# Optimization experiments

Measured on AMD Instinct MI355X. Metric: run time of the kernel, lower is better.

## Reference

```python
import jax, jax.numpy as jnp
import numpy as np

N = 50000
E = 800000
IN_DIM = 128
OUT_DIM = 64


def setup_inputs() -> dict:
    key = jax.random.key(0)
    ks = jax.random.split(key, 6)
    adj = jax.random.randint(ks[0], (2, E), 0, N)
    h = jax.random.normal(ks[1], (N, IN_DIM), dtype=jnp.float32)
    # fc: Linear(in_dim, out_dim) -> weight [out_dim, in_dim], bias [out_dim]
    W_fc = jax.random.normal(ks[2], (OUT_DIM, IN_DIM), dtype=jnp.float32) * (1.0 / np.sqrt(IN_DIM))
    b_fc = jnp.zeros((OUT_DIM,), dtype=jnp.float32)
    # attn_fc: Linear(2*out_dim, 1) -> weight [1, 2*out_dim], bias [1]
    W_att = jax.random.normal(ks[3], (1, 2 * OUT_DIM), dtype=jnp.float32) * (1.0 / np.sqrt(2 * OUT_DIM))
    b_att = jnp.zeros((1,), dtype=jnp.float32)
    return {"adj": adj, "h": h, "W_fc": W_fc, "b_fc": b_fc, "W_att": W_att, "b_att": b_att}


def reference(adj, h, W_fc, b_fc, W_att, b_att):
    # z = fc(h): [N, out_dim]
    z = h @ W_fc.T + b_fc
    src = adj[0]
    dst = adj[1]
    z_src = z[src]  # [E, out_dim]
    z_dst = z[dst]  # [E, out_dim]
    # attn_fc(cat(z_src, z_dst)) == z_src @ W1 + z_dst @ W2 + b; avoid explicit concat split
    w1 = W_att[0, :OUT_DIM]
    w2 = W_att[0, OUT_DIM:]
    att_logit = z_src @ w1 + z_dst @ w2 + b_att[0]  # [E]
    att_edge = jax.nn.leaky_relu(att_logit, negative_slope=0.01)[:, None]  # [E, 1]
    # scatter-add weighted source features to destination nodes
    out = jax.ops.segment_sum(z_src * att_edge, dst, num_segments=N)  # [N, out_dim]
    return out
```

## Files before the change

### kernel.cpp

```cpp
#include <hip/hip_runtime.h>
#include <hip/hip_bf16.h>

#define N_NODES 50000
#define E_EDGES 800000
#define IN_DIM  128
#define OUT_DIM 64
#define MTILES  (N_NODES / 16)
#define NB      196
#define BCAP    6144
#define OVF_CAP 16384
#define NBLK_FC 782
#define NBLK_SA 625
#define EPA     1280
#define ITER_A  5

static_assert(N_NODES % 16 == 0, "16-row MFMA tiles");
static_assert(N_NODES < 65536, "node ids packed in 16 bits");
static_assert(NBLK_SA * EPA == E_EDGES, "pass-A blocks partition edges");
static_assert(EPA == ITER_A * 256, "uniform per-thread trip count");
static_assert(NB * 256 >= N_NODES, "buckets cover dst space");


typedef __attribute__((ext_vector_type(8))) short bf16x8;
typedef __attribute__((ext_vector_type(4))) float f32x4;
typedef __attribute__((ext_vector_type(8))) unsigned short u16x8;

__device__ __forceinline__ unsigned short f32_to_bf16_rne(float f) {
    unsigned u = __float_as_uint(f);
    return (unsigned short)((u + 0x7FFFu + ((u >> 16) & 1u)) >> 16);
}
__device__ __forceinline__ float bf16_to_f32(unsigned short s) {
    return __uint_as_float(((unsigned)s) << 16);
}

__global__ __launch_bounds__(256) void gat_fc_scatter(
    const float* __restrict__ h,
    const float* __restrict__ Wfc,
    const float* __restrict__ bfc,
    const float* __restrict__ Watt,
    const float* __restrict__ batt,
    const int*   __restrict__ adj,
    unsigned short* __restrict__ z16,
    float* __restrict__ s1,
    float* __restrict__ s2,
    int*      __restrict__ gcnt,
    unsigned* __restrict__ coarse,
    unsigned* __restrict__ ovf)
{
    __shared__ short Wlds[OUT_DIM][IN_DIM + 8];

    if (blockIdx.x < NBLK_FC) {
        for (int i = threadIdx.x; i < OUT_DIM * IN_DIM; i += 256) {
            const int o = i >> 7;
            const int k = i & 127;
            Wlds[o][k] = (short)f32_to_bf16_rne(Wfc[i]);
        }
        __syncthreads();

        const int lane  = threadIdx.x & 63;
        const int c     = lane & 15;
        const int q     = lane >> 4;
        const int mtile = blockIdx.x * 4 + (threadIdx.x >> 6);
        if (mtile >= MTILES) return;
        const int n0 = mtile * 16;

        bf16x8 B[4][4];
        #pragma unroll
        for (int t = 0; t < 4; ++t)
            #pragma unroll
            for (int f = 0; f < 4; ++f)
                B[t][f] = *(const bf16x8*)&Wlds[f * 16 + c][t * 32 + q * 8];

        f32x4 acc[4] = {{0,0,0,0},{0,0,0,0},{0,0,0,0},{0,0,0,0}};

        const float* arow = h + (size_t)(n0 + c) * IN_DIM + q * 8;
        #pragma unroll
        for (int t = 0; t < 4; ++t) {
            float4 x0 = *(const float4*)(arow + t * 32);
            float4 x1 = *(const float4*)(arow + t * 32 + 4);
            bf16x8 a;
            a[0] = (short)f32_to_bf16_rne(x0.x);
            a[1] = (short)f32_to_bf16_rne(x0.y);
            a[2] = (short)f32_to_bf16_rne(x0.z);
            a[3] = (short)f32_to_bf16_rne(x0.w);
            a[4] = (short)f32_to_bf16_rne(x1.x);
            a[5] = (short)f32_to_bf16_rne(x1.y);
            a[6] = (short)f32_to_bf16_rne(x1.z);
            a[7] = (short)f32_to_bf16_rne(x1.w);
            #pragma unroll
            for (int f = 0; f < 4; ++f)
                acc[f] = __builtin_amdgcn_mfma_f32_16x16x32_bf16(a, B[t][f], acc[f], 0, 0, 0);
        }

        const float batt0 = batt[0];
        float w1c[4], w2c[4], bv[4];
        #pragma unroll
        for (int f = 0; f < 4; ++f) {
            w1c[f] = Watt[f * 16 + c];
            w2c[f] = Watt[OUT_DIM + f * 16 + c];
            bv[f]  = bfc[f * 16 + c];
        }
        float p1[4] = {0,0,0,0}, p2[4] = {0,0,0,0};
        #pragma unroll
        for (int f = 0; f < 4; ++f)
            #pragma unroll
            for (int r = 0; r < 4; ++r) {
                const float v = acc[f][r] + bv[f];
                z16[(size_t)(n0 + q * 4 + r) * OUT_DIM + f * 16 + c] = f32_to_bf16_rne(v);
                p1[r] += v * w1c[f];
                p2[r] += v * w2c[f];
            }
        #pragma unroll
        for (int r = 0; r < 4; ++r) {
            #pragma unroll
            for (int off = 1; off < 16; off <<= 1) {
                p1[r] += __shfl_xor(p1[r], off, 64);
                p2[r] += __shfl_xor(p2[r], off, 64);
            }
            if (c == 0) {
                s1[n0 + q * 4 + r] = p1[r];
                s2[n0 + q * 4 + r] = p2[r] + batt0;
            }
        }
    } else {
        __shared__ unsigned el[EPA];
        __shared__ int sof[256];
        __shared__ int bexc[NB], lcur[NB], gbase[NB];

        const int k  = blockIdx.x - NBLK_FC;
        const int e0 = k * EPA;
        const int t  = threadIdx.x;

        sof[t] = 0;
        __syncthreads();

        unsigned dv[ITER_A], sv[ITER_A];
        #pragma unroll
        for (int it = 0; it < ITER_A; ++it) {
            dv[it] = (unsigned)adj[E_EDGES + e0 + t + it * 256];
            sv[it] = (unsigned)adj[e0 + t + it * 256];
        }

        #pragma unroll
        for (int it = 0; it < ITER_A; ++it)
            atomicAdd(&sof[dv[it] >> 8], 1);
        __syncthreads();
        const int v = sof[t];
        __syncthreads();

        sof[t] = v;
        __syncthreads();
        #pragma unroll
        for (int o = 1; o < 256; o <<= 1) {
            const int add = (t >= o) ? sof[t - o] : 0;
            __syncthreads();
            sof[t] += add;
            __syncthreads();
        }
        if (t < NB) {
            const int excl = sof[t] - v;
            bexc[t]  = excl;
            lcur[t]  = excl;
            gbase[t] = atomicAdd(&gcnt[t], v);
        }
        __syncthreads();

        #pragma unroll
        for (int it = 0; it < ITER_A; ++it) {
            const int b = (int)(dv[it] >> 8);
            const int p = atomicAdd(&lcur[b], 1);
            el[p] = (dv[it] << 16) | sv[it];
        }
        __syncthreads();

        #pragma unroll
        for (int it = 0; it < ITER_A; ++it) {
            const int i = t + it * 256;
            const unsigned packed = el[i];
            const int b = (int)(packed >> 24);
            const int pin = gbase[b] + (i - bexc[b]);
            if (pin < BCAP) {
                coarse[(size_t)b * BCAP + pin] = packed;
            } else {
                const int o = atomicAdd(&gcnt[NB], 1);
                if (o < OVF_CAP) ovf[o] = packed;
            }
        }
    }
}

__global__ __launch_bounds__(512) void gat_binsort(
    unsigned* __restrict__ coarse,
    const int* __restrict__ gcnt,
    int* __restrict__ start, int* __restrict__ deg)
{
    __shared__ unsigned el[BCAP];
    __shared__ int hist[256], sof[256], cur[256];
    const int b  = blockIdx.x;
    const int t  = threadIdx.x;
    const int nb = min(gcnt[b], BCAP);

    if (t < 256) hist[t] = 0;
    __syncthreads();

    #pragma unroll 4
    for (int i = t; i < nb; i += 512) {
        const unsigned e = coarse[(size_t)b * BCAP + i];
        el[i] = e;
        atomicAdd(&hist[(e >> 16) & 255], 1);
    }
    __syncthreads();

    const int v = (t < 256) ? hist[t] : 0;
    if (t < 256) sof[t] = v;
    __syncthreads();
    #pragma unroll
    for (int o = 1; o < 256; o <<= 1) {
        const int add = (t >= o && t < 256) ? sof[t - o] : 0;
        __syncthreads();
        if (t < 256) sof[t] += add;
        __syncthreads();
    }
    if (t < 256) {
        const int excl = sof[t] - v;
        cur[t] = excl;
        const int n = b * 256 + t;
        if (n < N_NODES) {
            start[n] = b * BCAP + excl;
            deg[n]   = v;
        }
    }
    __syncthreads();

    #pragma unroll 4
    for (int i = t; i < nb; i += 512) {
        const unsigned e = el[i];
        const int p = atomicAdd(&cur[(e >> 16) & 255], 1);
        coarse[(size_t)b * BCAP + p] = e;
    }
}

__global__ __launch_bounds__(256) void gat_gather(
    const int* __restrict__ start, const int* __restrict__ deg,
    const unsigned* __restrict__ coarse, const int* __restrict__ gcnt,
    const unsigned* __restrict__ ovf,
    const float* __restrict__ s1, const float* __restrict__ s2,
    const unsigned short* __restrict__ z16,
    float* __restrict__ out)
{
    const int lane = threadIdx.x & 63;
    const int c    = lane & 7;
    const int q    = lane >> 3;
    const int n    = blockIdx.x * 4 + (threadIdx.x >> 6);
    if (n >= N_NODES) return;

    const int m  = deg[n];
    const int jb = start[n];
    const float s2n = s2[n];

    float acc[8] = {0,0,0,0,0,0,0,0};
    int j = 0;
    for (; j + 16 <= m; j += 16) {
        const int srcA = (int)(coarse[jb + j + q] & 0xFFFFu);
        const int srcB = (int)(coarse[jb + j + 8 + q] & 0xFFFFu);
        float aA = s1[srcA] + s2n;
        float aB = s1[srcB] + s2n;
        aA = (aA > 0.f) ? aA : 0.01f * aA;
        aB = (aB > 0.f) ? aB : 0.01f * aB;
        const u16x8 zA = *(const u16x8*)&z16[(size_t)srcA * OUT_DIM + 8 * c];
        const u16x8 zB = *(const u16x8*)&z16[(size_t)srcB * OUT_DIM + 8 * c];
        #pragma unroll
        for (int t = 0; t < 8; ++t) acc[t] += aA * bf16_to_f32(zA[t]);
        #pragma unroll
        for (int t = 0; t < 8; ++t) acc[t] += aB * bf16_to_f32(zB[t]);
    }
    for (; j + 8 <= m; j += 8) {
        const int src = (int)(coarse[jb + j + q] & 0xFFFFu);
        float a = s1[src] + s2n;
        a = (a > 0.f) ? a : 0.01f * a;
        const u16x8 zz = *(const u16x8*)&z16[(size_t)src * OUT_DIM + 8 * c];
        #pragma unroll
        for (int t = 0; t < 8; ++t) acc[t] += a * bf16_to_f32(zz[t]);
    }
    if (q < m - j) {
        const int src = (int)(coarse[jb + j + q] & 0xFFFFu);
        float a = s1[src] + s2n;
        a = (a > 0.f) ? a : 0.01f * a;
        const u16x8 zz = *(const u16x8*)&z16[(size_t)src * OUT_DIM + 8 * c];
        #pragma unroll
        for (int t = 0; t < 8; ++t) acc[t] += a * bf16_to_f32(zz[t]);
    }

    const int novf = min(gcnt[NB], OVF_CAP);
    for (int base = 0; base < novf; base += 8) {
        const int idx = base + q;
        const unsigned packed = (idx < novf) ? ovf[idx] : 0xFFFFFFFFu;
        const bool valid = (idx < novf) && ((packed >> 16) == (unsigned)n);
        const int src = valid ? (int)(packed & 0xFFFFu) : 0;
        float a = s1[src] + s2n;
        a = (a > 0.f) ? a : 0.01f * a;
        a = valid ? a : 0.f;
        const u16x8 zz = *(const u16x8*)&z16[(size_t)src * OUT_DIM + 8 * c];
        #pragma unroll
        for (int t = 0; t < 8; ++t) acc[t] += a * bf16_to_f32(zz[t]);
    }

    #pragma unroll
    for (int t = 0; t < 8; ++t) {
        acc[t] += __shfl_xor(acc[t], 8, 64);
        acc[t] += __shfl_xor(acc[t], 16, 64);
        acc[t] += __shfl_xor(acc[t], 32, 64);
    }

    if (q == 0) {
        float4 lo = make_float4(acc[0], acc[1], acc[2], acc[3]);
        float4 hi = make_float4(acc[4], acc[5], acc[6], acc[7]);
        *(float4*)&out[(size_t)n * OUT_DIM + 8 * c]     = lo;
        *(float4*)&out[(size_t)n * OUT_DIM + 8 * c + 4] = hi;
    }
}

extern "C" void kernel_launch(void* const* d_in, const int* in_sizes, int n_in,
                              void* d_out, int out_size, void* d_ws, size_t ws_size,
                              hipStream_t stream)
{
    const int*   adj  = (const int*)  d_in[0];
    const float* h    = (const float*)d_in[1];
    const float* Wfc  = (const float*)d_in[2];
    const float* bfc  = (const float*)d_in[3];
    const float* Watt = (const float*)d_in[4];
    const float* batt = (const float*)d_in[5];
    float* out = (float*)d_out;

    unsigned short* z16 = (unsigned short*)d_ws;
    float* s1    = (float*)(z16 + (size_t)N_NODES * OUT_DIM);
    float* s2    = s1 + N_NODES;
    int*   start = (int*)(s2 + N_NODES);
    int*   deg   = start + N_NODES;
    int*   gcnt  = deg + N_NODES;
    unsigned* ovf    = (unsigned*)(gcnt + NB + 1);
    unsigned* coarse = ovf + OVF_CAP;

    hipMemsetAsync(gcnt, 0, (NB + 1) * sizeof(int), stream);

    gat_fc_scatter<<<NBLK_FC + NBLK_SA, 256, 0, stream>>>(
        h, Wfc, bfc, Watt, batt, adj, z16, s1, s2, gcnt, coarse, ovf);
    gat_binsort<<<NB, 512, 0, stream>>>(coarse, gcnt, start, deg);
    gat_gather<<<(N_NODES + 3) / 4, 256, 0, stream>>>(
        start, deg, coarse, gcnt, ovf, s1, s2, z16, out);
}
```

Baseline: 129.8 us.

## Fuse per-bucket bin sort with gather into one kernel using shared memory

Merges the bucket counting sort and the per-node gather into a single kernel. The sorted edge list, degrees and offsets stay in shared memory, so the global writes of start/deg and the re-sorted edge array are no longer needed, and one kernel launch is removed. In exchange the gather phase runs on only 196 blocks of 1024 threads, with each wave processing 16 destination nodes sequentially. This sharply lowers the parallelism and latency hiding available for the random z16 loads.

Result: no change. 131.9 us (+1.6%).

```diff
diff --git a/kernel.cpp b/kernel.cpp
--- a/kernel.cpp
+++ b/kernel.cpp
@@ -189,134 +189,127 @@
     }
 }
 
-__global__ __launch_bounds__(512) void gat_binsort(
-    unsigned* __restrict__ coarse,
+__global__ __launch_bounds__(1024) void gat_sort_gather(
+    const unsigned* __restrict__ coarse,
     const int* __restrict__ gcnt,
-    int* __restrict__ start, int* __restrict__ deg)
-{
-    __shared__ unsigned el[BCAP];
-    __shared__ int hist[256], sof[256], cur[256];
-    const int b  = blockIdx.x;
-    const int t  = threadIdx.x;
-    const int nb = min(gcnt[b], BCAP);
-
-    if (t < 256) hist[t] = 0;
-    __syncthreads();
-
-    #pragma unroll 4
-    for (int i = t; i < nb; i += 512) {
-        const unsigned e = coarse[(size_t)b * BCAP + i];
-        el[i] = e;
-        atomicAdd(&hist[(e >> 16) & 255], 1);
-    }
-    __syncthreads();
-
-    const int v = (t < 256) ? hist[t] : 0;
-    if (t < 256) sof[t] = v;
-    __syncthreads();
-    #pragma unroll
-    for (int o = 1; o < 256; o <<= 1) {
-        const int add = (t >= o && t < 256) ? sof[t - o] : 0;
-        __syncthreads();
-        if (t < 256) sof[t] += add;
-        __syncthreads();
-    }
-    if (t < 256) {
-        const int excl = sof[t] - v;
-        cur[t] = excl;
-        const int n = b * 256 + t;
-        if (n < N_NODES) {
-            start[n] = b * BCAP + excl;
-            deg[n]   = v;
-        }
-    }
-    __syncthreads();
-
-    #pragma unroll 4
-    for (int i = t; i < nb; i += 512) {
-        const unsigned e = el[i];
-        const int p = atomicAdd(&cur[(e >> 16) & 255], 1);
-        coarse[(size_t)b * BCAP + p] = e;
-    }
-}
-
-__global__ __launch_bounds__(256) void gat_gather(
-    const int* __restrict__ start, const int* __restrict__ deg,
-    const unsigned* __restrict__ coarse, const int* __restrict__ gcnt,
     const unsigned* __restrict__ ovf,
     const float* __restrict__ s1, const float* __restrict__ s2,
     const unsigned short* __restrict__ z16,
     float* __restrict__ out)
 {
-    const int lane = threadIdx.x & 63;
+    __shared__ unsigned el[BCAP];
+    __shared__ unsigned es[BCAP];
+    __shared__ int hist[256], sof[256], cur[256];
+    const int b  = blockIdx.x;
+    const int t  = threadIdx.x;
+    const int nb = min(gcnt[b], BCAP);
+
+    if (t < 256) hist[t] = 0;
+    __syncthreads();
+
+    #pragma unroll 2
+    for (int i = t; i < nb; i += 1024) {
+        const unsigned e = coarse[(size_t)b * BCAP + i];
+        el[i] = e;
+        atomicAdd(&hist[(e >> 16) & 255], 1);
+    }
+    __syncthreads();
+
+    const int v = (t < 256) ? hist[t] : 0;
+    if (t < 256) sof[t] = v;
+    __syncthreads();
+    #pragma unroll
+    for (int o = 1; o < 256; o <<= 1) {
+        const int add = (t >= o && t < 256) ? sof[t - o] : 0;
+        __syncthreads();
+        if (t < 256) sof[t] += add;
+        __syncthreads();
+    }
+    if (t < 256) cur[t] = sof[t] - v;
+    __syncthreads();
+
+    #pragma unroll 2
+    for (int i = t; i < nb; i += 1024) {
+        const unsigned e = el[i];
+        const int p = atomicAdd(&cur[(e >> 16) & 255], 1);
+        es[p] = e;
+    }
+    __syncthreads();
+
+    const int lane = t & 63;
     const int c    = lane & 7;
     const int q    = lane >> 3;
-    const int n    = blockIdx.x * 4 + (threadIdx.x >> 6);
-    if (n >= N_NODES) return;
-
-    const int m  = deg[n];
-    const int jb = start[n];
-    const float s2n = s2[n];
-
-    float acc[8] = {0,0,0,0,0,0,0,0};
-    int j = 0;
-    for (; j + 16 <= m; j += 16) {
-        const int srcA = (int)(coarse[jb + j + q] & 0xFFFFu);
-        const int srcB = (int)(coarse[jb + j + 8 + q] & 0xFFFFu);
-        float aA = s1[srcA] + s2n;
-        float aB = s1[srcB] + s2n;
-        aA = (aA > 0.f) ? aA : 0.01f * aA;
-        aB = (aB > 0.f) ? aB : 0.01f * aB;
-        const u16x8 zA = *(const u16x8*)&z16[(size_t)srcA * OUT_DIM + 8 * c];
-        const u16x8 zB = *(const u16x8*)&z16[(size_t)srcB * OUT_DIM + 8 * c];
-        #pragma unroll
-        for (int t = 0; t < 8; ++t) acc[t] += aA * bf16_to_f32(zA[t]);
-        #pragma unroll
-        for (int t = 0; t < 8; ++t) acc[t] += aB * bf16_to_f32(zB[t]);
-    }
-    for (; j + 8 <= m; j += 8) {
-        const int src = (int)(coarse[jb + j + q] & 0xFFFFu);
-        float a = s1[src] + s2n;
-        a = (a > 0.f) ? a : 0.01f * a;
-        const u16x8 zz = *(const u16x8*)&z16[(size_t)src * OUT_DIM + 8 * c];
-        #pragma unroll
-        for (int t = 0; t < 8; ++t) acc[t] += a * bf16_to_f32(zz[t]);
-    }
-    if (q < m - j) {
-        const int src = (int)(coarse[jb + j + q] & 0xFFFFu);
-        float a = s1[src] + s2n;
-        a = (a > 0.f) ? a : 0.01f * a;
-        const u16x8 zz = *(const u16x8*)&z16[(size_t)src * OUT_DIM + 8 * c];
-        #pragma unroll
-        for (int t = 0; t < 8; ++t) acc[t] += a * bf16_to_f32(zz[t]);
-    }
-
+    const int w    = t >> 6;
     const int novf = min(gcnt[NB], OVF_CAP);
-    for (int base = 0; base < novf; base += 8) {
-        const int idx = base + q;
-        const unsigned packed = (idx < novf) ? ovf[idx] : 0xFFFFFFFFu;
-        const bool valid = (idx < novf) && ((packed >> 16) == (unsigned)n);
-        const int src = valid ? (int)(packed & 0xFFFFu) : 0;
-        float a = s1[src] + s2n;
-        a = (a > 0.f) ? a : 0.01f * a;
-        a = valid ? a : 0.f;
-        const u16x8 zz = *(const u16x8*)&z16[(size_t)src * OUT_DIM + 8 * c];
-        #pragma unroll
-        for (int t = 0; t < 8; ++t) acc[t] += a * bf16_to_f32(zz[t]);
-    }
-
-    #pragma unroll
-    for (int t = 0; t < 8; ++t) {
-        acc[t] += __shfl_xor(acc[t], 8, 64);
-        acc[t] += __shfl_xor(acc[t], 16, 64);
-        acc[t] += __shfl_xor(acc[t], 32, 64);
-    }
-
-    if (q == 0) {
-        float4 lo = make_float4(acc[0], acc[1], acc[2], acc[3]);
-        float4 hi = make_float4(acc[4], acc[5], acc[6], acc[7]);
-        *(float4*)&out[(size_t)n * OUT_DIM + 8 * c]     = lo;
-        *(float4*)&out[(size_t)n * OUT_DIM + 8 * c + 4] = hi;
+
+    for (int i = 0; i < 16; ++i) {
+        const int ln = w * 16 + i;
+        const int n  = b * 256 + ln;
+        if (n >= N_NODES) continue;
+
+        const int m  = hist[ln];
+        const int jb = sof[ln] - m;
+        const float s2n = s2[n];
+
+        float acc[8] = {0,0,0,0,0,0,0,0};
+        int j = 0;
+        for (; j + 16 <= m; j += 16) {
+            const int srcA = (int)(es[jb + j + q] & 0xFFFFu);
+            const int srcB = (int)(es[jb + j + 8 + q] & 0xFFFFu);
+            float aA = s1[srcA] + s2n;
+            float aB = s1[srcB] + s2n;
+            aA = (aA > 0.f) ? aA : 0.01f * aA;
+            aB = (aB > 0.f) ? aB : 0.01f * aB;
+            const u16x8 zA = *(const u16x8*)&z16[(size_t)srcA * OUT_DIM + 8 * c];
+            const u16x8 zB = *(const u16x8*)&z16[(size_t)srcB * OUT_DIM + 8 * c];
+            #pragma unroll
+            for (int u = 0; u < 8; ++u) acc[u] += aA * bf16_to_f32(zA[u]);
+            #pragma unroll
+            for (int u = 0; u < 8; ++u) acc[u] += aB * bf16_to_f32(zB[u]);
+        }
+        for (; j + 8 <= m; j += 8) {
+            const int src = (int)(es[jb + j + q] & 0xFFFFu);
+            float a = s1[src] + s2n;
+            a = (a > 0.f) ? a : 0.01f * a;
+            const u16x8 zz = *(const u16x8*)&z16[(size_t)src * OUT_DIM + 8 * c];
+            #pragma unroll
+            for (int u = 0; u < 8; ++u) acc[u] += a * bf16_to_f32(zz[u]);
+        }
+        if (q < m - j) {
+            const int src = (int)(es[jb + j + q] & 0xFFFFu);
+            float a = s1[src] + s2n;
+            a = (a > 0.f) ? a : 0.01f * a;
+            const u16x8 zz = *(const u16x8*)&z16[(size_t)src * OUT_DIM + 8 * c];
+            #pragma unroll
+            for (int u = 0; u < 8; ++u) acc[u] += a * bf16_to_f32(zz[u]);
+        }
+
+        for (int base = 0; base < novf; base += 8) {
+            const int idx = base + q;
+            const unsigned packed = (idx < novf) ? ovf[idx] : 0xFFFFFFFFu;
+            const bool valid = (idx < novf) && ((packed >> 16) == (unsigned)n);
+            const int src = valid ? (int)(packed & 0xFFFFu) : 0;
+            float a = s1[src] + s2n;
+            a = (a > 0.f) ? a : 0.01f * a;
+            a = valid ? a : 0.f;
+            const u16x8 zz = *(const u16x8*)&z16[(size_t)src * OUT_DIM + 8 * c];
+            #pragma unroll
+            for (int u = 0; u < 8; ++u) acc[u] += a * bf16_to_f32(zz[u]);
+        }
+
+        #pragma unroll
+        for (int u = 0; u < 8; ++u) {
+            acc[u] += __shfl_xor(acc[u], 8, 64);
+            acc[u] += __shfl_xor(acc[u], 16, 64);
+            acc[u] += __shfl_xor(acc[u], 32, 64);
+        }
+
+        if (q == 0) {
+            float4 lo = make_float4(acc[0], acc[1], acc[2], acc[3]);
+            float4 hi = make_float4(acc[4], acc[5], acc[6], acc[7]);
+            *(float4*)&out[(size_t)n * OUT_DIM + 8 * c]     = lo;
+            *(float4*)&out[(size_t)n * OUT_DIM + 8 * c + 4] = hi;
+        }
     }
 }
 
@@ -335,9 +328,7 @@
     unsigned short* z16 = (unsigned short*)d_ws;
     float* s1    = (float*)(z16 + (size_t)N_NODES * OUT_DIM);
     float* s2    = s1 + N_NODES;
-    int*   start = (int*)(s2 + N_NODES);
-    int*   deg   = start + N_NODES;
-    int*   gcnt  = deg + N_NODES;
+    int*   gcnt  = (int*)(s2 + N_NODES);
     unsigned* ovf    = (unsigned*)(gcnt + NB + 1);
     unsigned* coarse = ovf + OVF_CAP;
 
@@ -345,7 +336,6 @@
 
     gat_fc_scatter<<<NBLK_FC + NBLK_SA, 256, 0, stream>>>(
         h, Wfc, bfc, Watt, batt, adj, z16, s1, s2, gcnt, coarse, ovf);
-    gat_binsort<<<NB, 512, 0, stream>>>(coarse, gcnt, start, deg);
-    gat_gather<<<(N_NODES + 3) / 4, 256, 0, stream>>>(
-        start, deg, coarse, gcnt, ovf, s1, s2, z16, out);
-}
+    gat_sort_gather<<<NB, 1024, 0, stream>>>(
+        coarse, gcnt, ovf, s1, s2, z16, out);
+}
```

## Replace global bucket atomics with fixed per-block slots compacted in binsort

Applied to the files above, without the earlier changes.

Each scatter block now writes its per-bucket edges into fixed 16-entry slots and records a per-block count, instead of reserving space through a global atomicAdd per bucket. The binsort kernel gathers the slots with wave-ballot compaction into shared memory and writes the sorted result to a separate buffer. The aim is to remove contention on the global bucket counters and one memset. In exchange, binsort must scan a larger, partly empty slot array. Edges beyond 16 per block-bucket, or beyond the bucket capacity, go to the overflow list, and the gather kernel now skips overflow batches with no matches using __any.

Measured after the change: 143.3 us. 1.1x slower.

```diff
diff --git a/kernel.cpp b/kernel.cpp
--- a/kernel.cpp
+++ b/kernel.cpp
@@ -13,6 +13,7 @@
 #define NBLK_SA 625
 #define EPA     1280
 #define ITER_A  5
+#define SLOTS   16
 
 static_assert(N_NODES % 16 == 0, "16-row MFMA tiles");
 static_assert(N_NODES < 65536, "node ids packed in 16 bits");
@@ -43,8 +44,9 @@
     unsigned short* __restrict__ z16,
     float* __restrict__ s1,
     float* __restrict__ s2,
-    int*      __restrict__ gcnt,
-    unsigned* __restrict__ coarse,
+    unsigned short* __restrict__ cnt,
+    unsigned* __restrict__ craw,
+    int*      __restrict__ ovfc,
     unsigned* __restrict__ ovf)
 {
     __shared__ short Wlds[OUT_DIM][IN_DIM + 8];
@@ -125,7 +127,7 @@
     } else {
         __shared__ unsigned el[EPA];
         __shared__ int sof[256];
-        __shared__ int bexc[NB], lcur[NB], gbase[NB];
+        __shared__ int bexc[NB], lcur[NB];
 
         const int k  = blockIdx.x - NBLK_FC;
         const int e0 = k * EPA;
@@ -159,9 +161,9 @@
         }
         if (t < NB) {
             const int excl = sof[t] - v;
-            bexc[t]  = excl;
-            lcur[t]  = excl;
-            gbase[t] = atomicAdd(&gcnt[t], v);
+            bexc[t] = excl;
+            lcur[t] = excl;
+            cnt[(size_t)t * NBLK_SA + k] = (unsigned short)min(v, SLOTS);
         }
         __syncthreads();
 
@@ -178,11 +180,11 @@
             const int i = t + it * 256;
             const unsigned packed = el[i];
             const int b = (int)(packed >> 24);
-            const int pin = gbase[b] + (i - bexc[b]);
-            if (pin < BCAP) {
-                coarse[(size_t)b * BCAP + pin] = packed;
+            const int p = i - bexc[b];
+            if (p < SLOTS) {
+                craw[((size_t)b * NBLK_SA + k) * SLOTS + p] = packed;
             } else {
-                const int o = atomicAdd(&gcnt[NB], 1);
+                const int o = atomicAdd(ovfc, 1);
                 if (o < OVF_CAP) ovf[o] = packed;
             }
         }
@@ -190,26 +192,51 @@
 }
 
 __global__ __launch_bounds__(512) void gat_binsort(
-    unsigned* __restrict__ coarse,
-    const int* __restrict__ gcnt,
-    int* __restrict__ start, int* __restrict__ deg)
+    const unsigned* __restrict__ craw,
+    const unsigned short* __restrict__ cnt,
+    unsigned* __restrict__ csrt,
+    int* __restrict__ start, int* __restrict__ deg,
+    int* __restrict__ ovfc, unsigned* __restrict__ ovf)
 {
     __shared__ unsigned el[BCAP];
     __shared__ int hist[256], sof[256], cur[256];
-    const int b  = blockIdx.x;
-    const int t  = threadIdx.x;
-    const int nb = min(gcnt[b], BCAP);
+    __shared__ unsigned short cl[NBLK_SA];
+    __shared__ int ncur;
+    const int b = blockIdx.x;
+    const int t = threadIdx.x;
+    const int lane = t & 63;
 
     if (t < 256) hist[t] = 0;
+    if (t == 0) ncur = 0;
+    for (int i = t; i < NBLK_SA; i += 512) cl[i] = cnt[(size_t)b * NBLK_SA + i];
     __syncthreads();
 
-    #pragma unroll 4
-    for (int i = t; i < nb; i += 512) {
-        const unsigned e = coarse[(size_t)b * BCAP + i];
-        el[i] = e;
-        atomicAdd(&hist[(e >> 16) & 255], 1);
+    for (int i = t; i < NBLK_SA * SLOTS; i += 512) {
+        const int blk = i >> 4;
+        const int s   = i & (SLOTS - 1);
+        const bool act = s < (int)cl[blk];
+        unsigned e = 0u;
+        if (act) e = craw[(size_t)b * (NBLK_SA * SLOTS) + i];
+        const unsigned long long m = __ballot(act);
+        if (m != 0ull) {
+            const int ldr = (int)__builtin_ctzll(m);
+            int wbase = 0;
+            if (lane == ldr) wbase = atomicAdd(&ncur, (int)__popcll(m));
+            wbase = __shfl(wbase, ldr, 64);
+            if (act) {
+                const int p = wbase + (int)__popcll(m & ((1ull << lane) - 1ull));
+                if (p < BCAP) {
+                    el[p] = e;
+                    atomicAdd(&hist[(e >> 16) & 255], 1);
+                } else {
+                    const int o = atomicAdd(ovfc, 1);
+                    if (o < OVF_CAP) ovf[o] = e;
+                }
+            }
+        }
     }
     __syncthreads();
+    const int nb = min(ncur, BCAP);
 
     const int v = (t < 256) ? hist[t] : 0;
     if (t < 256) sof[t] = v;
@@ -236,13 +263,13 @@
     for (int i = t; i < nb; i += 512) {
         const unsigned e = el[i];
         const int p = atomicAdd(&cur[(e >> 16) & 255], 1);
-        coarse[(size_t)b * BCAP + p] = e;
+        csrt[(size_t)b * BCAP + p] = e;
     }
 }
 
 __global__ __launch_bounds__(256) void gat_gather(
     const int* __restrict__ start, const int* __restrict__ deg,
-    const unsigned* __restrict__ coarse, const int* __restrict__ gcnt,
+    const unsigned* __restrict__ csrt, const int* __restrict__ ovfc,
     const unsigned* __restrict__ ovf,
     const float* __restrict__ s1, const float* __restrict__ s2,
     const unsigned short* __restrict__ z16,
@@ -261,8 +288,8 @@
     float acc[8] = {0,0,0,0,0,0,0,0};
     int j = 0;
     for (; j + 16 <= m; j += 16) {
-        const int srcA = (int)(coarse[jb + j + q] & 0xFFFFu);
-        const int srcB = (int)(coarse[jb + j + 8 + q] & 0xFFFFu);
+        const int srcA = (int)(csrt[jb + j + q] & 0xFFFFu);
+        const int srcB = (int)(csrt[jb + j + 8 + q] & 0xFFFFu);
         float aA = s1[srcA] + s2n;
         float aB = s1[srcB] + s2n;
         aA = (aA > 0.f) ? aA : 0.01f * aA;
@@ -270,46 +297,48 @@
         const u16x8 zA = *(const u16x8*)&z16[(size_t)srcA * OUT_DIM + 8 * c];
         const u16x8 zB = *(const u16x8*)&z16[(size_t)srcB * OUT_DIM + 8 * c];
         #pragma unroll
-        for (int t = 0; t < 8; ++t) acc[t] += aA * bf16_to_f32(zA[t]);
-        #pragma unroll
-        for (int t = 0; t < 8; ++t) acc[t] += aB * bf16_to_f32(zB[t]);
+        for (int u = 0; u < 8; ++u) acc[u] += aA * bf16_to_f32(zA[u]);
+        #pragma unroll
+        for (int u = 0; u < 8; ++u) acc[u] += aB * bf16_to_f32(zB[u]);
     }
     for (; j + 8 <= m; j += 8) {
-        const int src = (int)(coarse[jb + j + q] & 0xFFFFu);
+        const int src = (int)(csrt[jb + j + q] & 0xFFFFu);
         float a = s1[src] + s2n;
         a = (a > 0.f) ? a : 0.01f * a;
         const u16x8 zz = *(const u16x8*)&z16[(size_t)src * OUT_DIM + 8 * c];
         #pragma unroll
-        for (int t = 0; t < 8; ++t) acc[t] += a * bf16_to_f32(zz[t]);
+        for (int u = 0; u < 8; ++u) acc[u] += a * bf16_to_f32(zz[u]);
     }
     if (q < m - j) {
-        const int src = (int)(coarse[jb + j + q] & 0xFFFFu);
+        const int src = (int)(csrt[jb + j + q] & 0xFFFFu);
         float a = s1[src] + s2n;
         a = (a > 0.f) ? a : 0.01f * a;
         const u16x8 zz = *(const u16x8*)&z16[(size_t)src * OUT_DIM + 8 * c];
         #pragma unroll
-        for (int t = 0; t < 8; ++t) acc[t] += a * bf16_to_f32(zz[t]);
-    }
-
-    const int novf = min(gcnt[NB], OVF_CAP);
+        for (int u = 0; u < 8; ++u) acc[u] += a * bf16_to_f32(zz[u]);
+    }
+
+    const int novf = min(ovfc[0], OVF_CAP);
     for (int base = 0; base < novf; base += 8) {
         const int idx = base + q;
         const unsigned packed = (idx < novf) ? ovf[idx] : 0xFFFFFFFFu;
         const bool valid = (idx < novf) && ((packed >> 16) == (unsigned)n);
-        const int src = valid ? (int)(packed & 0xFFFFu) : 0;
-        float a = s1[src] + s2n;
-        a = (a > 0.f) ? a : 0.01f * a;
-        a = valid ? a : 0.f;
-        const u16x8 zz = *(const u16x8*)&z16[(size_t)src * OUT_DIM + 8 * c];
-        #pragma unroll
-        for (int t = 0; t < 8; ++t) acc[t] += a * bf16_to_f32(zz[t]);
+        if (__any(valid)) {
+            const int src = valid ? (int)(packed & 0xFFFFu) : 0;
+            float a = s1[src] + s2n;
+            a = (a > 0.f) ? a : 0.01f * a;
+            a = valid ? a : 0.f;
+            const u16x8 zz = *(const u16x8*)&z16[(size_t)src * OUT_DIM + 8 * c];
+            #pragma unroll
+            for (int u = 0; u < 8; ++u) acc[u] += a * bf16_to_f32(zz[u]);
+        }
     }
 
     #pragma unroll
-    for (int t = 0; t < 8; ++t) {
-        acc[t] += __shfl_xor(acc[t], 8, 64);
-        acc[t] += __shfl_xor(acc[t], 16, 64);
-        acc[t] += __shfl_xor(acc[t], 32, 64);
+    for (int u = 0; u < 8; ++u) {
+        acc[u] += __shfl_xor(acc[u], 8, 64);
+        acc[u] += __shfl_xor(acc[u], 16, 64);
+        acc[u] += __shfl_xor(acc[u], 32, 64);
     }
 
     if (q == 0) {
@@ -337,15 +366,17 @@
     float* s2    = s1 + N_NODES;
     int*   start = (int*)(s2 + N_NODES);
     int*   deg   = start + N_NODES;
-    int*   gcnt  = deg + N_NODES;
-    unsigned* ovf    = (unsigned*)(gcnt + NB + 1);
-    unsigned* coarse = ovf + OVF_CAP;
-
-    hipMemsetAsync(gcnt, 0, (NB + 1) * sizeof(int), stream);
+    int*   ovfc  = deg + N_NODES;
+    unsigned* ovf = (unsigned*)(ovfc + 1);
+    unsigned short* cnt = (unsigned short*)(ovf + OVF_CAP);
+    unsigned* craw = (unsigned*)(cnt + (size_t)NB * NBLK_SA);
+    unsigned* csrt = craw + (size_t)NB * NBLK_SA * SLOTS;
+
+    hipMemsetAsync(ovfc, 0, sizeof(int), stream);
 
     gat_fc_scatter<<<NBLK_FC + NBLK_SA, 256, 0, stream>>>(
-        h, Wfc, bfc, Watt, batt, adj, z16, s1, s2, gcnt, coarse, ovf);
-    gat_binsort<<<NB, 512, 0, stream>>>(coarse, gcnt, start, deg);
+        h, Wfc, bfc, Watt, batt, adj, z16, s1, s2, cnt, craw, ovfc, ovf);
+    gat_binsort<<<NB, 512, 0, stream>>>(craw, cnt, csrt, start, deg, ovfc, ovf);
     gat_gather<<<(N_NODES + 3) / 4, 256, 0, stream>>>(
-        start, deg, coarse, gcnt, ovf, s1, s2, z16, out);
-}
+        start, deg, csrt, ovfc, ovf, s1, s2, z16, out);
+}
```
